# Kernel tuning notes

Measured on AMD Instinct MI355X. Metric: run time of the kernel, lower is better.

The kernel has to match this reference:

```python
import jax, jax.numpy as jnp
import numpy as np

B, S, D = 4096, 200, 64
EPS = 1e-3  # keras BatchNormalization default epsilon

def setup_inputs() -> dict:
    key = jax.random.key(0)
    ks = jax.random.split(key, 8)
    return {
        "em": jax.random.normal(ks[0], (B, D), jnp.float32),
        "eu": jax.random.normal(ks[1], (B, D), jnp.float32),
        "Xu": jax.random.normal(ks[2], (B, S, D), jnp.float32),
        "W1": jax.random.normal(ks[3], (4 * D, 64), jnp.float32) * 0.05,
        "b1": jnp.zeros((64,), jnp.float32),
        "W2": jax.random.normal(ks[4], (64, 32), jnp.float32) * 0.1,
        "b2": jnp.zeros((32,), jnp.float32),
        "W3": jax.random.normal(ks[5], (32, 1), jnp.float32) * 0.1,
        "b3": jnp.zeros((1,), jnp.float32),
        "gamma": jnp.ones((2 * D,), jnp.float32),
        "beta": jnp.zeros((2 * D,), jnp.float32),
        "mov_mean": jnp.zeros((2 * D,), jnp.float32),
        "mov_var": jnp.ones((2 * D,), jnp.float32),
    }

def reference(em, eu, Xu, W1, b1, W2, b2, W3, b3, gamma, beta, mov_mean, mov_var):
    # DIN attention: query = em tiled over seq, key = value = Xu
    q = jnp.broadcast_to(em[:, None, :], Xu.shape)            # [B,S,D]
    info = jnp.concatenate([q, Xu, q - Xu, q * Xu], axis=-1)  # [B,S,4D]
    h = jax.nn.relu(info @ W1 + b1)                           # [B,S,64]
    h = jax.nn.relu(h @ W2 + b2)                              # [B,S,32]
    logits = (h @ W3 + b3)[..., 0]                            # [B,S]
    w = jax.nn.softmax(logits, axis=-1)                       # [B,S]
    pooled = jnp.einsum('bs,bsd->bd', w, Xu)                  # [B,D]
    info_all = jnp.concatenate([pooled, em], axis=-1)         # [B,2D]
    bn = (info_all - mov_mean) * jax.lax.rsqrt(mov_var + EPS) * gamma + beta
    return jnp.concatenate([bn, eu], axis=-1)                 # [B,2D+Du]
```

## Files before the change

### kernel.cpp

```cpp
#include <hip/hip_runtime.h>
#include <hip/hip_bf16.h>
#include <math.h>

typedef __bf16 bf16_t;
typedef bf16_t bf16x4 __attribute__((ext_vector_type(4)));
typedef bf16_t bf16x8 __attribute__((ext_vector_type(8)));
typedef float  f32x4  __attribute__((ext_vector_type(4)));

#define SEQ 200
#define SP  208
#define DD  64
#define RS  72

#define MFMA(a, b, c) __builtin_amdgcn_mfma_f32_16x16x32_bf16((a), (b), (c), 0, 0, 0)

__global__ __launch_bounds__(256) void prep_kernel(
    const float* __restrict__ em, const float* __restrict__ W1,
    const float* __restrict__ b1, const float* __restrict__ W2,
    bf16_t* __restrict__ Wbc, bf16_t* __restrict__ W1dt,
    bf16_t* __restrict__ W2t, float* __restrict__ Q)
{
  const int tid = threadIdx.x;
  if (blockIdx.x == 0) {
    for (int i = tid; i < 64 * 64; i += 256) {
      int n = i >> 6, k = i & 63;
      Wbc[i]  = (bf16_t)(W1[(64 + k) * 64 + n] - W1[(128 + k) * 64 + n]);
      W1dt[i] = (bf16_t)(W1[(192 + k) * 64 + n]);
    }
    for (int i = tid; i < 32 * 64; i += 256) {
      int n = i >> 6, k = i & 63;
      W2t[i] = (bf16_t)(W2[k * 32 + n]);
    }
  } else {
    int b = (blockIdx.x - 1) * 4 + (tid >> 6);
    int n = tid & 63;
    float acc = b1[n];
    for (int d = 0; d < 64; ++d)
      acc += em[(size_t)b * 64 + d] * (W1[d * 64 + n] + W1[(128 + d) * 64 + n]);
    Q[(size_t)b * 64 + n] = acc;
  }
}

__global__ __launch_bounds__(256, 4) void din_kernel(
    const float* __restrict__ em, const float* __restrict__ eu,
    const float* __restrict__ Xu, const float* __restrict__ b2,
    const float* __restrict__ W3, const float* __restrict__ b3,
    const float* __restrict__ gam, const float* __restrict__ bet,
    const float* __restrict__ mmean, const float* __restrict__ mvar,
    const bf16_t* __restrict__ Wbc, const bf16_t* __restrict__ W1dt,
    const bf16_t* __restrict__ W2t, const float* __restrict__ Q,
    float* __restrict__ out)
{
  __shared__ __align__(16) bf16_t A[SP * RS];
  __shared__ float logits[SP];
  __shared__ float red[8];
  float* part = (float*)A;

  const int tid  = threadIdx.x;
  const int b    = blockIdx.x;
  const int lane = tid & 63;
  const int wid  = tid >> 6;
  const int g    = lane >> 4;
  const int l16  = lane & 15;
  const int n1   = 16 * wid + l16;

  for (int i = tid; i < 8 * DD; i += 256) {
    int r = SEQ + (i >> 6), c = i & 63;
    A[r * RS + c] = (bf16_t)0.f;
  }

  const bf16x8* Wbc8  = (const bf16x8*)Wbc;
  const bf16x8* W1dt8 = (const bf16x8*)W1dt;
  const bf16x8* W2t8  = (const bf16x8*)W2t;
  bf16x8 bB[2];
  #pragma unroll
  for (int c = 0; c < 2; ++c) {
    bf16x8 wbc = Wbc8[n1 * 8 + 4 * c + g];
    bf16x8 w1d = W1dt8[n1 * 8 + 4 * c + g];
    float4 e0 = *(const float4*)&em[(size_t)b * DD + 32 * c + 8 * g];
    float4 e1 = *(const float4*)&em[(size_t)b * DD + 32 * c + 8 * g + 4];
    bB[c][0] = (bf16_t)((float)wbc[0] + e0.x * (float)w1d[0]);
    bB[c][1] = (bf16_t)((float)wbc[1] + e0.y * (float)w1d[1]);
    bB[c][2] = (bf16_t)((float)wbc[2] + e0.z * (float)w1d[2]);
    bB[c][3] = (bf16_t)((float)wbc[3] + e0.w * (float)w1d[3]);
    bB[c][4] = (bf16_t)((float)wbc[4] + e1.x * (float)w1d[4]);
    bB[c][5] = (bf16_t)((float)wbc[5] + e1.y * (float)w1d[5]);
    bB[c][6] = (bf16_t)((float)wbc[6] + e1.z * (float)w1d[6]);
    bB[c][7] = (bf16_t)((float)wbc[7] + e1.w * (float)w1d[7]);
  }
  bf16x8 bW2f[2][2];
  #pragma unroll
  for (int c = 0; c < 2; ++c)
    #pragma unroll
    for (int u = 0; u < 2; ++u)
      bW2f[c][u] = W2t8[(16 * u + l16) * 8 + 4 * c + g];

  const float qn   = Q[(size_t)b * DD + n1];
  const float b2v0 = b2[l16], b2v1 = b2[16 + l16];
  const float w3v0 = W3[l16], w3v1 = W3[16 + l16];
  const float b3s  = b3[0];

  const float4* Xr = (const float4*)(Xu + (size_t)b * SEQ * DD);
  bf16x4 xr[13];
  #pragma unroll
  for (int k = 0; k < 13; ++k) {
    int v = tid + 256 * k;
    if (v < SEQ * DD / 4) {
      int s  = v >> 4;
      int c4 = (v & 15) * 4;
      float4 x = Xr[v];
      bf16x4 xa;
      xa[0] = (bf16_t)x.x; xa[1] = (bf16_t)x.y;
      xa[2] = (bf16_t)x.z; xa[3] = (bf16_t)x.w;
      xr[k] = xa;
      *(bf16x4*)&A[s * RS + c4] = xa;
    } else {
      xr[k][0] = (bf16_t)0.f; xr[k][1] = (bf16_t)0.f;
      xr[k][2] = (bf16_t)0.f; xr[k][3] = (bf16_t)0.f;
    }
  }
  __syncthreads();

  for (int t = 0; t < 13; ++t) {
    int rb = (16 * t + l16) * RS + 8 * g;
    bf16x8 a0 = *(const bf16x8*)&A[rb];
    bf16x8 a1 = *(const bf16x8*)&A[rb + 32];
    f32x4 a = {0.f, 0.f, 0.f, 0.f};
    a = MFMA(a0, bB[0], a);
    a = MFMA(a1, bB[1], a);
    __syncthreads();
    #pragma unroll
    for (int r = 0; r < 4; ++r) {
      float v = a[r] + qn;
      v = v > 0.f ? v : 0.f;
      A[(16 * t + 4 * g + r) * RS + n1] = (bf16_t)v;
    }
  }
  __syncthreads();

  for (int t = wid; t < 13; t += 4) {
    int rb = (16 * t + l16) * RS + 8 * g;
    bf16x8 h0 = *(const bf16x8*)&A[rb];
    bf16x8 h1 = *(const bf16x8*)&A[rb + 32];
    f32x4 a0 = {0.f, 0.f, 0.f, 0.f}, a1 = {0.f, 0.f, 0.f, 0.f};
    a0 = MFMA(h0, bW2f[0][0], a0);
    a0 = MFMA(h1, bW2f[1][0], a0);
    a1 = MFMA(h0, bW2f[0][1], a1);
    a1 = MFMA(h1, bW2f[1][1], a1);
    #pragma unroll
    for (int r = 0; r < 4; ++r) {
      float p0 = fmaxf(a0[r] + b2v0, 0.f) * w3v0;
      float p1 = fmaxf(a1[r] + b2v1, 0.f) * w3v1;
      float pr = p0 + p1;
      pr += __shfl_xor(pr, 1);
      pr += __shfl_xor(pr, 2);
      pr += __shfl_xor(pr, 4);
      pr += __shfl_xor(pr, 8);
      if (l16 == 0) logits[16 * t + 4 * g + r] = pr + b3s;
    }
  }
  __syncthreads();

  float lv = (tid < SEQ) ? logits[tid] : -INFINITY;
  float mx = lv;
  #pragma unroll
  for (int o = 32; o > 0; o >>= 1) mx = fmaxf(mx, __shfl_xor(mx, o));
  if (lane == 0) red[wid] = mx;
  __syncthreads();
  mx = fmaxf(fmaxf(red[0], red[1]), fmaxf(red[2], red[3]));
  float e = (tid < SEQ) ? __expf(lv - mx) : 0.f;
  float ssum = e;
  #pragma unroll
  for (int o = 32; o > 0; o >>= 1) ssum += __shfl_xor(ssum, o);
  if (lane == 0) red[4 + wid] = ssum;
  __syncthreads();
  float inv = 1.f / (red[4] + red[5] + red[6] + red[7]);
  if (tid < SEQ) logits[tid] = e * inv;
  __syncthreads();

  {
    float4 ps = {0.f, 0.f, 0.f, 0.f};
    #pragma unroll
    for (int k = 0; k < 13; ++k) {
      int v = tid + 256 * k;
      if (v < SEQ * DD / 4) {
        float w = logits[(tid >> 4) + 16 * k];
        ps.x += w * (float)xr[k][0];
        ps.y += w * (float)xr[k][1];
        ps.z += w * (float)xr[k][2];
        ps.w += w * (float)xr[k][3];
      }
    }
    *(float4*)&part[(tid >> 4) * 68 + (tid & 15) * 4] = ps;
  }
  __syncthreads();

  if (tid < 192) {
    float v;
    if (tid < 128) {
      float x;
      if (tid < 64) {
        x = 0.f;
        #pragma unroll
        for (int r = 0; r < 16; ++r) x += part[r * 68 + tid];
      } else {
        x = em[(size_t)b * DD + (tid - 64)];
      }
      v = (x - mmean[tid]) * rsqrtf(mvar[tid] + 1e-3f) * gam[tid] + bet[tid];
    } else {
      v = eu[(size_t)b * DD + (tid - 128)];
    }
    out[(size_t)b * 192 + tid] = v;
  }
}

extern "C" void kernel_launch(void* const* d_in, const int* in_sizes, int n_in,
                              void* d_out, int out_size, void* d_ws, size_t ws_size,
                              hipStream_t stream) {
  const float* em = (const float*)d_in[0];
  const float* eu = (const float*)d_in[1];
  const float* Xu = (const float*)d_in[2];
  const float* W1 = (const float*)d_in[3];
  const float* b1 = (const float*)d_in[4];
  const float* W2 = (const float*)d_in[5];
  const float* b2 = (const float*)d_in[6];
  const float* W3 = (const float*)d_in[7];
  const float* b3 = (const float*)d_in[8];
  const float* ga = (const float*)d_in[9];
  const float* be = (const float*)d_in[10];
  const float* mm = (const float*)d_in[11];
  const float* mv = (const float*)d_in[12];
  int B = in_sizes[0] / DD;

  float*  Q    = (float*)d_ws;
  bf16_t* Wbc  = (bf16_t*)((char*)d_ws + (size_t)B * 64 * 4);
  bf16_t* W1dt = Wbc  + 64 * 64;
  bf16_t* W2t  = W1dt + 64 * 64;

  prep_kernel<<<1 + B / 4, 256, 0, stream>>>(em, W1, b1, W2, Wbc, W1dt, W2t, Q);
  din_kernel<<<B, 256, 0, stream>>>(em, eu, Xu, b2, W3, b3, ga, be, mm, mv,
                                    Wbc, W1dt, W2t, Q, (float*)d_out);
}
```

Baseline: 332.6 us.

## Hoist Xu loads early, batch layer-1 MFMAs, and remove barriers

All 13 float4 loads of Xu are now issued at the start of the kernel, before the weight and bias setup, so global memory latency overlaps that setup. The first-layer MFMAs for all 13 tiles are computed into registers with one barrier before the results are written back to LDS, replacing a barrier per tile. The softmax normalization is folded into the pooling weights, which removes one more barrier, and the W2 fragment load is deferred to reduce register pressure. In exchange, the kernel holds 13 float4 and 13 f32x4 values in registers, which may hurt occupancy at the 4-blocks-per-CU launch bound.

```diff
diff --git a/kernel.cpp b/kernel.cpp
--- a/kernel.cpp
+++ b/kernel.cpp
@@ -69,6 +69,12 @@
     A[r * RS + c] = (bf16_t)0.f;
   }
 
+  const float4* Xr = (const float4*)(Xu + (size_t)b * SEQ * DD);
+  float4 xg[13];
+  #pragma unroll
+  for (int k = 0; k < 12; ++k) xg[k] = Xr[tid + 256 * k];
+  xg[12] = (tid < 128) ? Xr[tid + 3072] : make_float4(0.f, 0.f, 0.f, 0.f);
+
   const bf16x8* Wbc8  = (const bf16x8*)Wbc;
   const bf16x8* W1dt8 = (const bf16x8*)W1dt;
   const bf16x8* W2t8  = (const bf16x8*)W2t;
@@ -88,39 +94,26 @@
     bB[c][6] = (bf16_t)((float)wbc[6] + e1.z * (float)w1d[6]);
     bB[c][7] = (bf16_t)((float)wbc[7] + e1.w * (float)w1d[7]);
   }
-  bf16x8 bW2f[2][2];
-  #pragma unroll
-  for (int c = 0; c < 2; ++c)
-    #pragma unroll
-    for (int u = 0; u < 2; ++u)
-      bW2f[c][u] = W2t8[(16 * u + l16) * 8 + 4 * c + g];
-
   const float qn   = Q[(size_t)b * DD + n1];
   const float b2v0 = b2[l16], b2v1 = b2[16 + l16];
   const float w3v0 = W3[l16], w3v1 = W3[16 + l16];
   const float b3s  = b3[0];
 
-  const float4* Xr = (const float4*)(Xu + (size_t)b * SEQ * DD);
   bf16x4 xr[13];
   #pragma unroll
   for (int k = 0; k < 13; ++k) {
+    bf16x4 xa;
+    xa[0] = (bf16_t)xg[k].x; xa[1] = (bf16_t)xg[k].y;
+    xa[2] = (bf16_t)xg[k].z; xa[3] = (bf16_t)xg[k].w;
+    xr[k] = xa;
     int v = tid + 256 * k;
-    if (v < SEQ * DD / 4) {
-      int s  = v >> 4;
-      int c4 = (v & 15) * 4;
-      float4 x = Xr[v];
-      bf16x4 xa;
-      xa[0] = (bf16_t)x.x; xa[1] = (bf16_t)x.y;
-      xa[2] = (bf16_t)x.z; xa[3] = (bf16_t)x.w;
-      xr[k] = xa;
-      *(bf16x4*)&A[s * RS + c4] = xa;
-    } else {
-      xr[k][0] = (bf16_t)0.f; xr[k][1] = (bf16_t)0.f;
-      xr[k][2] = (bf16_t)0.f; xr[k][3] = (bf16_t)0.f;
-    }
-  }
-  __syncthreads();
-
+    if (v < SEQ * DD / 4)
+      *(bf16x4*)&A[(v >> 4) * RS + (v & 15) * 4] = xa;
+  }
+  __syncthreads();
+
+  f32x4 acc[13];
+  #pragma unroll
   for (int t = 0; t < 13; ++t) {
     int rb = (16 * t + l16) * RS + 8 * g;
     bf16x8 a0 = *(const bf16x8*)&A[rb];
@@ -128,15 +121,26 @@
     f32x4 a = {0.f, 0.f, 0.f, 0.f};
     a = MFMA(a0, bB[0], a);
     a = MFMA(a1, bB[1], a);
-    __syncthreads();
+    acc[t] = a;
+  }
+  __syncthreads();
+
+  #pragma unroll
+  for (int t = 0; t < 13; ++t)
     #pragma unroll
     for (int r = 0; r < 4; ++r) {
-      float v = a[r] + qn;
+      float v = acc[t][r] + qn;
       v = v > 0.f ? v : 0.f;
       A[(16 * t + 4 * g + r) * RS + n1] = (bf16_t)v;
     }
-  }
-  __syncthreads();
+  __syncthreads();
+
+  bf16x8 bW2f[2][2];
+  #pragma unroll
+  for (int c = 0; c < 2; ++c)
+    #pragma unroll
+    for (int u = 0; u < 2; ++u)
+      bW2f[c][u] = W2t8[(16 * u + l16) * 8 + 4 * c + g];
 
   for (int t = wid; t < 13; t += 4) {
     int rb = (16 * t + l16) * RS + 8 * g;
@@ -169,14 +173,13 @@
   __syncthreads();
   mx = fmaxf(fmaxf(red[0], red[1]), fmaxf(red[2], red[3]));
   float e = (tid < SEQ) ? __expf(lv - mx) : 0.f;
+  if (tid < SEQ) logits[tid] = e;
   float ssum = e;
   #pragma unroll
   for (int o = 32; o > 0; o >>= 1) ssum += __shfl_xor(ssum, o);
   if (lane == 0) red[4 + wid] = ssum;
   __syncthreads();
-  float inv = 1.f / (red[4] + red[5] + red[6] + red[7]);
-  if (tid < SEQ) logits[tid] = e * inv;
-  __syncthreads();
+  const float inv = 1.f / (red[4] + red[5] + red[6] + red[7]);
 
   {
     float4 ps = {0.f, 0.f, 0.f, 0.f};
@@ -184,7 +187,7 @@
     for (int k = 0; k < 13; ++k) {
       int v = tid + 256 * k;
       if (v < SEQ * DD / 4) {
-        float w = logits[(tid >> 4) + 16 * k];
+        float w = logits[(tid >> 4) + 16 * k] * inv;
         ps.x += w * (float)xr[k][0];
         ps.y += w * (float)xr[k][1];
         ps.z += w * (float)xr[k][2];
```

Measured after the change: 326.5 us. No clear change (-1.8%).
